# Kernel tuning notes

Measured on AMD Instinct MI355X. Metric: run time of the kernel, lower is better.

Reference implementation:

```python
import jax, jax.numpy as jnp
import numpy as np
import math

IN_C = 768
CA = 384
K1 = (3, 1, 1)
K2 = (1, 3, 3)
K3 = (3, 3, 3)


def _dwconv3d(x, w, b):
    # x: [B, Ca, T, H, W]; w: [Ca, 1, kt, kh, kw]; depthwise (groups = Ca)
    pads = [(k // 2, k // 2) for k in w.shape[2:]]
    y = jax.lax.conv_general_dilated(
        x, w, window_strides=(1, 1, 1), padding=pads,
        feature_group_count=x.shape[1],
        dimension_numbers=("NCDHW", "OIDHW", "NCDHW"))
    return y + b[None, :, None, None, None]


def setup_inputs() -> dict:
    key = jax.random.key(0)
    ks = jax.random.split(key, 12)
    s = 0.02
    x = jax.random.normal(ks[0], (128, 197, IN_C), dtype=jnp.float32)
    fc1_w = jax.random.normal(ks[1], (CA, IN_C), dtype=jnp.float32) * s
    fc1_b = jnp.zeros((CA,), dtype=jnp.float32)
    conv1_w = jax.random.normal(ks[2], (CA, 1) + K1, dtype=jnp.float32) * s
    conv1_b = jax.random.normal(ks[3], (CA,), dtype=jnp.float32) * s
    conv2_w = jax.random.normal(ks[4], (CA, 1) + K2, dtype=jnp.float32) * s
    conv2_b = jax.random.normal(ks[5], (CA,), dtype=jnp.float32) * s
    conv3_w = jax.random.normal(ks[6], (CA, 1) + K3, dtype=jnp.float32) * s
    conv3_b = jax.random.normal(ks[7], (CA,), dtype=jnp.float32) * s
    proj_w = jax.random.normal(ks[8], (CA, 1) + K1, dtype=jnp.float32) * s
    proj_b = jax.random.normal(ks[9], (CA,), dtype=jnp.float32) * s
    fc2_w = jax.random.normal(ks[10], (IN_C, CA), dtype=jnp.float32) * s
    fc2_b = jnp.zeros((IN_C,), dtype=jnp.float32)
    return {
        "x": x, "fc1_w": fc1_w, "fc1_b": fc1_b,
        "conv1_w": conv1_w, "conv1_b": conv1_b,
        "conv2_w": conv2_w, "conv2_b": conv2_b,
        "conv3_w": conv3_w, "conv3_b": conv3_b,
        "proj_w": proj_w, "proj_b": proj_b,
        "fc2_w": fc2_w, "fc2_b": fc2_b,
        "T": 16,
    }


def reference(x, fc1_w, fc1_b, conv1_w, conv1_b, conv2_w, conv2_b,
              conv3_w, conv3_b, proj_w, proj_b, fc2_w, fc2_b, T):
    BT, L, C = x.shape
    B = BT // T
    H = W = round(math.sqrt(L - 1))
    Ca = fc1_w.shape[0]
    x_id = x
    # drop CLS token, project down: [BT, L-1, Ca]
    h = jnp.einsum("blc,ac->bla", x[:, 1:, :], fc1_w) + fc1_b
    # [B, Ca, T, H, W]
    h = h.reshape(B, T, H, W, Ca).transpose(0, 4, 1, 2, 3)
    identity = h
    h = (_dwconv3d(h, conv1_w, conv1_b)
         + _dwconv3d(h, conv2_w, conv2_b)
         + _dwconv3d(h, conv3_w, conv3_b)) / 3.0
    h = h + identity
    h = h + _dwconv3d(h, proj_w, proj_b)
    # back to tokens: [BT, L-1, Ca]
    h = h.transpose(0, 2, 3, 4, 1).reshape(BT, L - 1, Ca)
    h = jnp.einsum("bla,ca->blc", h, fc2_w) + fc2_b
    return x_id.at[:, 1:, :].add(h)
```

## Files before the change

kernel.cpp:

```cpp
#include <hip/hip_runtime.h>
#include <cstdint>

typedef __bf16 bf16_t;
typedef __bf16 bf16x4 __attribute__((ext_vector_type(4)));
typedef __bf16 bf16x8 __attribute__((ext_vector_type(8)));
typedef float f32x4 __attribute__((ext_vector_type(4)));

#define BT_   128
#define LTOK  197
#define CIN   768
#define CA_   384
#define TT    16
#define HH    14
#define NTOK  25088

__device__ __forceinline__ void gl_lds16(const void* g, void* l) {
  __builtin_amdgcn_global_load_lds(
      (const __attribute__((address_space(1))) unsigned int*)g,
      (__attribute__((address_space(3))) unsigned int*)l,
      16, 0, 0);
}

#define SBAR() do { __builtin_amdgcn_sched_barrier(0); \
                    __builtin_amdgcn_s_barrier(); \
                    __builtin_amdgcn_sched_barrier(0); } while (0)

__global__ void prep_weights_kernel(
    const float* __restrict__ c1w, const float* __restrict__ c1b,
    const float* __restrict__ c2w, const float* __restrict__ c2b,
    const float* __restrict__ c3w, const float* __restrict__ c3b,
    const float* __restrict__ projw,
    bf16_t* __restrict__ Wtb,
    float* __restrict__ beff,
    float* __restrict__ pwt) {
  int a = blockIdx.x * blockDim.x + threadIdx.x;
  if (a >= CA_) return;
  for (int dt = 0; dt < 3; dt++)
    for (int dh = 0; dh < 3; dh++)
      for (int dw = 0; dw < 3; dw++) {
        float v = c3w[a*27 + dt*9 + dh*3 + dw];
        if (dh == 1 && dw == 1) v += c1w[a*3 + dt];
        if (dt == 1)            v += c2w[a*9 + dh*3 + dw];
        v *= (1.0f/3.0f);
        if (dt == 1 && dh == 1 && dw == 1) v += 1.0f;
        Wtb[((dt*3+dh)*3+dw)*CA_ + a] = (bf16_t)v;
      }
  beff[a] = (c1b[a] + c2b[a] + c3b[a]) * (1.0f/3.0f);
  pwt[0*CA_ + a] = projw[a*3 + 0];
  pwt[1*CA_ + a] = projw[a*3 + 1];
  pwt[2*CA_ + a] = projw[a*3 + 2];
}

__global__ __launch_bounds__(256) void convert_w_kernel(
    const float* __restrict__ fc1w, const float* __restrict__ fc2w,
    const float* __restrict__ x, float* __restrict__ out,
    bf16_t* __restrict__ W1f, bf16_t* __restrict__ W2f,
    bf16_t* __restrict__ xb) {
  const int NW1 = CA_*CIN/4;
  const int NW2 = CIN*CA_/4;
  const int NX  = BT_*LTOK*CIN/4;
  const int total = NW1 + NW2 + NX;
  for (int i = blockIdx.x*256 + threadIdx.x; i < total; i += gridDim.x*256) {
    if (i < NW1) {
      int e = i*4, f = e >> 9, t = e & 511, l = t >> 3, jb = t & 7;
      int ch = f / 24, cb = f - ch*24;
      int col = cb*16 + (l & 15);
      int k   = ch*32 + ((l >> 4) << 3) + jb;
      float4 v = *(const float4*)(fc1w + (size_t)col*CIN + k);
      bf16x4 b; b[0]=(bf16_t)v.x; b[1]=(bf16_t)v.y; b[2]=(bf16_t)v.z; b[3]=(bf16_t)v.w;
      *(bf16x4*)(W1f + e) = b;
    } else if (i < NW1 + NW2) {
      int e = (i - NW1)*4, f = e >> 9, t = e & 511, l = t >> 3, jb = t & 7;
      int ch = f / 48, cb = f - ch*48;
      int col = cb*16 + (l & 15);
      int k   = ch*32 + ((l >> 4) << 3) + jb;
      float4 v = *(const float4*)(fc2w + (size_t)col*CA_ + k);
      bf16x4 b; b[0]=(bf16_t)v.x; b[1]=(bf16_t)v.y; b[2]=(bf16_t)v.z; b[3]=(bf16_t)v.w;
      *(bf16x4*)(W2f + e) = b;
    } else {
      int j = i - NW1 - NW2;
      int row = j / 192;
      int c4  = j - row*192;
      int l   = row % 197;
      float4 v = ((const float4*)x)[(size_t)j];
      if (l == 0) {
        ((float4*)out)[(size_t)j] = v;
      } else {
        int tok = (row/197)*196 + (l - 1);
        bf16x4 b; b[0]=(bf16_t)v.x; b[1]=(bf16_t)v.y; b[2]=(bf16_t)v.z; b[3]=(bf16_t)v.w;
        *(bf16x4*)(xb + (size_t)tok*CIN + c4*4) = b;
      }
    }
  }
}

__global__ __launch_bounds__(256) void gemm1_kernel(
    const bf16_t* __restrict__ xb, const bf16_t* __restrict__ W1f,
    const float* __restrict__ fc1b, bf16_t* __restrict__ H0) {
  __shared__ bf16_t Alds[3][4096];
  const int tid  = threadIdx.x;
  const int lane = tid & 63;
  const int wave = tid >> 6;
  const int bm = blockIdx.x, bn = blockIdx.y;

  const bf16_t* asrc0 = xb + (size_t)(bm*128 + (tid>>2))*CIN + (tid&3)*8;
  const bf16_t* asrc1 = asrc0 + (size_t)64*CIN;
  const int off0 = tid*8;
  const int off1 = tid*8 + 2048;

  const int quad = lane >> 4;
  const int r16  = lane & 15;
  const int wm = (wave >> 1) * 64;
  const int wn = (wave & 1) * 64;

  const bf16_t* wb = W1f + ((size_t)(bn*8 + (wave & 1)*4))*512 + lane*8;

  f32x4 acc[4][4] = {};

#define G1_A(S, K) do { \
    gl_lds16(asrc0 + (K), &Alds[S][off0]); \
    gl_lds16(asrc1 + (K), &Alds[S][off1]); } while (0)
#define G1_B(CH) do { \
    bfr[0] = *(const bf16x8*)(wb + (size_t)((CH)*24 + 0)*512); \
    bfr[1] = *(const bf16x8*)(wb + (size_t)((CH)*24 + 1)*512); \
    bfr[2] = *(const bf16x8*)(wb + (size_t)((CH)*24 + 2)*512); \
    bfr[3] = *(const bf16x8*)(wb + (size_t)((CH)*24 + 3)*512); } while (0)
#define G1_M(S) do { bf16x8 af_[4]; \
    _Pragma("unroll") \
    for (int mt = 0; mt < 4; mt++) \
      af_[mt] = *(const bf16x8*)&Alds[S][(wm + mt*16 + r16)*32 + quad*8]; \
    _Pragma("unroll") \
    for (int mt = 0; mt < 4; mt++) \
      _Pragma("unroll") \
      for (int nt = 0; nt < 4; nt++) \
        acc[mt][nt] = __builtin_amdgcn_mfma_f32_16x16x32_bf16(af_[mt], bfr[nt], acc[mt][nt], 0, 0, 0); \
  } while (0)

  G1_A(0, 0);
  G1_A(1, 32);
  asm volatile("s_waitcnt vmcnt(2)" ::: "memory");
  SBAR();

  #pragma unroll 1
  for (int ii = 0; ii < 7; ii++) {
    #pragma unroll
    for (int j = 0; j < 3; j++) {
      const int i = ii*3 + j;
      bf16x8 bfr[4];
      G1_B(i);
      __builtin_amdgcn_sched_barrier(0);
      G1_A((j + 2) % 3, (i + 2)*32);
      G1_M(j);
      asm volatile("s_waitcnt vmcnt(2)" ::: "memory");
      SBAR();
    }
  }
  {
    bf16x8 bfr[4];
    G1_B(21);
    __builtin_amdgcn_sched_barrier(0);
    G1_A(2, 23*32);
    G1_M(0);
    asm volatile("s_waitcnt vmcnt(2)" ::: "memory");
    SBAR();
  }
  {
    bf16x8 bfr[4];
    G1_B(22);
    __builtin_amdgcn_sched_barrier(0);
    G1_M(1);
    asm volatile("s_waitcnt vmcnt(0)" ::: "memory");
    SBAR();
  }
  {
    bf16x8 bfr[4];
    G1_B(23);
    G1_M(2);
  }

  #pragma unroll
  for (int nt = 0; nt < 4; nt++) {
    const int col = bn*128 + wn + nt*16 + r16;
    const float bias = fc1b[col];
    #pragma unroll
    for (int mt = 0; mt < 4; mt++) {
      const int row0 = bm*128 + wm + mt*16 + quad*4;
      #pragma unroll
      for (int rg = 0; rg < 4; rg++)
        H0[(size_t)(row0 + rg)*CA_ + col] = (bf16_t)(acc[mt][nt][rg] + bias);
    }
  }
#undef G1_A
#undef G1_B
#undef G1_M
}

__global__ __launch_bounds__(192) void conv_kernel(
    const bf16_t* __restrict__ H0,
    const bf16_t* __restrict__ Wtb,
    const float* __restrict__ beff,
    const float* __restrict__ pwt,
    const float* __restrict__ pb,
    bf16_t* __restrict__ Z) {
  __shared__ bf16_t Wlds[27*CA_];
  __shared__ float  ybuf[2][2][CA_];

  const int tid = threadIdx.x;
  {
    const uint4* src = (const uint4*)Wtb;
    uint4* dst = (uint4*)Wlds;
    #pragma unroll
    for (int i = 0; i < 7; i++) {
      int idx = tid + i*192;
      if (idx < 27*CA_/8) dst[idx] = src[idx];
    }
  }

  const int blk  = blockIdx.x;
  const int b    = blk & 7;
  const int pair = blk >> 3;
  const int cg   = tid % 48;
  const int ct   = tid / 48;
  const int col  = ct >> 1;
  const int th   = ct & 1;
  const int hw   = pair*2 + col;
  const int h    = hw / HH, w = hw % HH;
  const int c0   = cg * 8;
  const int t0   = th * 8;

  float y[8][8];
  {
    f32x4 bv0 = *(const f32x4*)(beff + c0);
    f32x4 bv1 = *(const f32x4*)(beff + c0 + 4);
    #pragma unroll
    for (int i = 0; i < 8; i++) {
      #pragma unroll
      for (int c = 0; c < 4; c++) { y[i][c] = bv0[c]; y[i][c+4] = bv1[c]; }
    }
  }

  __syncthreads();

  const size_t rowstride = (size_t)196*CA_;
  const bf16_t* base_t0 = H0 + ((size_t)(b*TT + t0)*196)*CA_ + c0;
  const int tau_e_off = th ? -1 : 8;

  for (int j = 0; j < 9; j++) {
    const int dh = j / 3, dw = j - dh*3;
    const int h2 = h + dh - 1, w2 = w + dw - 1;
    const bool ok = ((unsigned)h2 < HH) && ((unsigned)w2 < HH);
    const int sp = ok ? (h2*HH + w2) : hw;
    const float m = ok ? 1.0f : 0.0f;

    const bf16x8 wv0 = *(const bf16x8*)&Wlds[(0*9+j)*CA_ + c0];
    const bf16x8 wv1 = *(const bf16x8*)&Wlds[(1*9+j)*CA_ + c0];
    const bf16x8 wv2 = *(const bf16x8*)&Wlds[(2*9+j)*CA_ + c0];
    float mw0[8], mw1[8], mw2[8];
    #pragma unroll
    for (int c = 0; c < 8; c++) {
      mw0[c] = m * (float)wv0[c];
      mw1[c] = m * (float)wv1[c];
      mw2[c] = m * (float)wv2[c];
    }

    const bf16_t* tp = base_t0 + (size_t)sp*CA_;
    bf16x8 gv[8];
    #pragma unroll
    for (int i = 0; i < 8; i++)
      gv[i] = *(const bf16x8*)(tp + (ptrdiff_t)i*(ptrdiff_t)rowstride);
    const bf16x8 ge = *(const bf16x8*)(tp + (ptrdiff_t)tau_e_off*(ptrdiff_t)rowstride);

    #pragma unroll
    for (int i = 0; i < 8; i++) {
      float gf[8];
      #pragma unroll
      for (int c = 0; c < 8; c++) gf[c] = (float)gv[i][c];
      #pragma unroll
      for (int c = 0; c < 8; c++) y[i][c] += gf[c]*mw1[c];
      if (i > 0) {
        #pragma unroll
        for (int c = 0; c < 8; c++) y[i-1][c] += gf[c]*mw2[c];
      }
      if (i < 7) {
        #pragma unroll
        for (int c = 0; c < 8; c++) y[i+1][c] += gf[c]*mw0[c];
      }
    }
    {
      float gf[8];
      #pragma unroll
      for (int c = 0; c < 8; c++) gf[c] = (float)ge[c];
      if (th) {
        #pragma unroll
        for (int c = 0; c < 8; c++) y[0][c] += gf[c]*mw0[c];
      } else {
        #pragma unroll
        for (int c = 0; c < 8; c++) y[7][c] += gf[c]*mw2[c];
      }
    }
  }

  #pragma unroll
  for (int c = 0; c < 8; c++) ybuf[col][th][c0+c] = th ? y[0][c] : y[7][c];
  __syncthreads();
  float yedge[8];
  #pragma unroll
  for (int c = 0; c < 8; c++) yedge[c] = ybuf[col][1-th][c0+c];

  float p0[8], p1[8], p2[8], pbv[8];
  {
    f32x4 a0 = *(const f32x4*)(pwt + 0*CA_ + c0), a1 = *(const f32x4*)(pwt + 0*CA_ + c0 + 4);
    f32x4 b0 = *(const f32x4*)(pwt + 1*CA_ + c0), b1 = *(const f32x4*)(pwt + 1*CA_ + c0 + 4);
    f32x4 d0 = *(const f32x4*)(pwt + 2*CA_ + c0), d1 = *(const f32x4*)(pwt + 2*CA_ + c0 + 4);
    f32x4 e0 = *(const f32x4*)(pb + c0),          e1 = *(const f32x4*)(pb + c0 + 4);
    #pragma unroll
    for (int c = 0; c < 4; c++) {
      p0[c]=a0[c]; p0[c+4]=a1[c];
      p1[c]=b0[c]; p1[c+4]=b1[c];
      p2[c]=d0[c]; p2[c+4]=d1[c];
      pbv[c]=e0[c]; pbv[c+4]=e1[c];
    }
  }

  bf16_t* zbase = Z + ((size_t)(b*TT + t0)*196 + hw)*CA_ + c0;
  #pragma unroll
  for (int i = 0; i < 8; i++) {
    bf16x8 zo;
    #pragma unroll
    for (int c = 0; c < 8; c++) {
      const float ym = (i > 0) ? y[i-1][c] : (th ? yedge[c] : 0.f);
      const float yp = (i < 7) ? y[i+1][c] : (th ? 0.f : yedge[c]);
      const float z  = y[i][c] + pbv[c] + p0[c]*ym + p1[c]*y[i][c] + p2[c]*yp;
      zo[c] = (bf16_t)z;
    }
    *(bf16x8*)(zbase + (size_t)i*rowstride) = zo;
  }
}

__global__ __launch_bounds__(256) void gemm2_kernel(
    const bf16_t* __restrict__ Z, const bf16_t* __restrict__ W2f,
    const float* __restrict__ fc2b, const float* __restrict__ x,
    float* __restrict__ out) {
  __shared__ bf16_t Alds[3][4096];
  const int tid  = threadIdx.x;
  const int lane = tid & 63;
  const int wave = tid >> 6;
  const int bm = blockIdx.x, bn = blockIdx.y;

  const bf16_t* asrc0 = Z + (size_t)(bm*128 + (tid>>2))*CA_ + (tid&3)*8;
  const bf16_t* asrc1 = asrc0 + (size_t)64*CA_;
  const int off0 = tid*8;
  const int off1 = tid*8 + 2048;

  const int quad = lane >> 4;
  const int r16  = lane & 15;
  const int wm = (wave >> 1) * 64;
  const int wn = (wave & 1) * 64;

  const bf16_t* wb = W2f + ((size_t)(bn*8 + (wave & 1)*4))*512 + lane*8;

  f32x4 acc[4][4] = {};

#define G2_A(S, K) do { \
    gl_lds16(asrc0 + (K), &Alds[S][off0]); \
    gl_lds16(asrc1 + (K), &Alds[S][off1]); } while (0)
#define G2_B(CH) do { \
    bfr[0] = *(const bf16x8*)(wb + (size_t)((CH)*48 + 0)*512); \
    bfr[1] = *(const bf16x8*)(wb + (size_t)((CH)*48 + 1)*512); \
    bfr[2] = *(const bf16x8*)(wb + (size_t)((CH)*48 + 2)*512); \
    bfr[3] = *(const bf16x8*)(wb + (size_t)((CH)*48 + 3)*512); } while (0)
#define G2_M(S) do { bf16x8 af_[4]; \
    _Pragma("unroll") \
    for (int mt = 0; mt < 4; mt++) \
      af_[mt] = *(const bf16x8*)&Alds[S][(wm + mt*16 + r16)*32 + quad*8]; \
    _Pragma("unroll") \
    for (int mt = 0; mt < 4; mt++) \
      _Pragma("unroll") \
      for (int nt = 0; nt < 4; nt++) \
        acc[mt][nt] = __builtin_amdgcn_mfma_f32_16x16x32_bf16(af_[mt], bfr[nt], acc[mt][nt], 0, 0, 0); \
  } while (0)

  G2_A(0, 0);
  G2_A(1, 32);
  asm volatile("s_waitcnt vmcnt(2)" ::: "memory");
  SBAR();

  #pragma unroll 1
  for (int ii = 0; ii < 3; ii++) {
    #pragma unroll
    for (int j = 0; j < 3; j++) {
      const int i = ii*3 + j;
      bf16x8 bfr[4];
      G2_B(i);
      __builtin_amdgcn_sched_barrier(0);
      G2_A((j + 2) % 3, (i + 2)*32);
      G2_M(j);
      asm volatile("s_waitcnt vmcnt(2)" ::: "memory");
      SBAR();
    }
  }
  {
    bf16x8 bfr[4];
    G2_B(9);
    __builtin_amdgcn_sched_barrier(0);
    G2_A(2, 11*32);
    G2_M(0);
    asm volatile("s_waitcnt vmcnt(2)" ::: "memory");
    SBAR();
  }
  {
    bf16x8 bfr[4];
    G2_B(10);
    __builtin_amdgcn_sched_barrier(0);
    G2_M(1);
    asm volatile("s_waitcnt vmcnt(0)" ::: "memory");
    SBAR();
  }
  {
    bf16x8 bfr[4];
    G2_B(11);
    G2_M(2);
  }

  #pragma unroll
  for (int nt = 0; nt < 4; nt++) {
    const int col = bn*128 + wn + nt*16 + r16;
    const float bias = fc2b[col];
    #pragma unroll
    for (int mt = 0; mt < 4; mt++) {
      #pragma unroll
      for (int rg = 0; rg < 4; rg++) {
        const int tok = bm*128 + wm + mt*16 + quad*4 + rg;
        const int bt  = tok / 196;
        const size_t o = (size_t)(tok + bt + 1)*CIN + col;
        out[o] = x[o] + acc[mt][nt][rg] + bias;
      }
    }
  }
#undef G2_A
#undef G2_B
#undef G2_M
}

extern "C" void kernel_launch(void* const* d_in, const int* in_sizes, int n_in,
                              void* d_out, int out_size, void* d_ws, size_t ws_size,
                              hipStream_t stream) {
  (void)in_sizes; (void)n_in; (void)out_size; (void)ws_size;
  const float* x    = (const float*)d_in[0];
  const float* fc1w = (const float*)d_in[1];
  const float* fc1b = (const float*)d_in[2];
  const float* c1w  = (const float*)d_in[3];
  const float* c1b  = (const float*)d_in[4];
  const float* c2w  = (const float*)d_in[5];
  const float* c2b  = (const float*)d_in[6];
  const float* c3w  = (const float*)d_in[7];
  const float* c3b  = (const float*)d_in[8];
  const float* pw   = (const float*)d_in[9];
  const float* pb   = (const float*)d_in[10];
  const float* fc2w = (const float*)d_in[11];
  const float* fc2b = (const float*)d_in[12];
  float* out = (float*)d_out;

  char* ws = (char*)d_ws;
  bf16_t* W1f  = (bf16_t*)(ws);
  bf16_t* W2f  = (bf16_t*)(ws + 589824);
  bf16_t* Wtb  = (bf16_t*)(ws + 1179648);
  float*  beff = (float*) (ws + 1200384);
  float*  pwt  = (float*) (ws + 1201920);
  bf16_t* xb   = (bf16_t*)(ws + 1206528);
  bf16_t* Z    = (bf16_t*)(ws + 1206528);
  bf16_t* H0   = (bf16_t*)(ws + 39741696);

  prep_weights_kernel<<<dim3(2), dim3(192), 0, stream>>>(
      c1w, c1b, c2w, c2b, c3w, c3b, pw, Wtb, beff, pwt);
  convert_w_kernel<<<dim3(4096), dim3(256), 0, stream>>>(fc1w, fc2w, x, out, W1f, W2f, xb);
  gemm1_kernel<<<dim3(196, 3), dim3(256), 0, stream>>>(xb, W1f, fc1b, H0);
  conv_kernel<<<dim3(784), dim3(192), 0, stream>>>(H0, Wtb, beff, pwt, pb, Z);
  gemm2_kernel<<<dim3(196, 6), dim3(256), 0, stream>>>(Z, W2f, fc2b, x, out);
}
```

Measured before the change: 266.3 us.

## Shrink GEMM block tiles to 64x128 and fold weight prep into convert kernel

Both GEMM kernels move from a 128x128 block tile (2x2 wave grid, 4x4 MFMA tiles per wave) to a 64x128 tile where each of the four waves owns 64 rows by 32 columns. This doubles the grid to 392 row blocks and halves LDS per block, aiming at better occupancy and load balance across CUs. The cost is more redundant B-weight loads and less A reuse per block. Separately, the small prep_weights kernel is merged into convert_w_kernel to save one launch.

After: 262.6 us. Within noise of the previous version (-1.4%).

```diff
diff --git a/kernel.cpp b/kernel.cpp
--- a/kernel.cpp
+++ b/kernel.cpp
@@ -25,42 +25,40 @@
                     __builtin_amdgcn_s_barrier(); \
                     __builtin_amdgcn_sched_barrier(0); } while (0)
 
-__global__ void prep_weights_kernel(
+__global__ __launch_bounds__(256) void convert_w_kernel(
+    const float* __restrict__ fc1w, const float* __restrict__ fc2w,
+    const float* __restrict__ x, float* __restrict__ out,
+    bf16_t* __restrict__ W1f, bf16_t* __restrict__ W2f,
+    bf16_t* __restrict__ xb,
     const float* __restrict__ c1w, const float* __restrict__ c1b,
     const float* __restrict__ c2w, const float* __restrict__ c2b,
     const float* __restrict__ c3w, const float* __restrict__ c3b,
     const float* __restrict__ projw,
-    bf16_t* __restrict__ Wtb,
-    float* __restrict__ beff,
-    float* __restrict__ pwt) {
-  int a = blockIdx.x * blockDim.x + threadIdx.x;
-  if (a >= CA_) return;
-  for (int dt = 0; dt < 3; dt++)
-    for (int dh = 0; dh < 3; dh++)
-      for (int dw = 0; dw < 3; dw++) {
-        float v = c3w[a*27 + dt*9 + dh*3 + dw];
-        if (dh == 1 && dw == 1) v += c1w[a*3 + dt];
-        if (dt == 1)            v += c2w[a*9 + dh*3 + dw];
-        v *= (1.0f/3.0f);
-        if (dt == 1 && dh == 1 && dw == 1) v += 1.0f;
-        Wtb[((dt*3+dh)*3+dw)*CA_ + a] = (bf16_t)v;
-      }
-  beff[a] = (c1b[a] + c2b[a] + c3b[a]) * (1.0f/3.0f);
-  pwt[0*CA_ + a] = projw[a*3 + 0];
-  pwt[1*CA_ + a] = projw[a*3 + 1];
-  pwt[2*CA_ + a] = projw[a*3 + 2];
-}
-
-__global__ __launch_bounds__(256) void convert_w_kernel(
-    const float* __restrict__ fc1w, const float* __restrict__ fc2w,
-    const float* __restrict__ x, float* __restrict__ out,
-    bf16_t* __restrict__ W1f, bf16_t* __restrict__ W2f,
-    bf16_t* __restrict__ xb) {
+    bf16_t* __restrict__ Wtb, float* __restrict__ beff, float* __restrict__ pwt) {
+  const int gid = blockIdx.x*256 + threadIdx.x;
+  if (gid < CA_) {
+    const int a = gid;
+    for (int dt = 0; dt < 3; dt++)
+      for (int dh = 0; dh < 3; dh++)
+        for (int dw = 0; dw < 3; dw++) {
+          float v = c3w[a*27 + dt*9 + dh*3 + dw];
+          if (dh == 1 && dw == 1) v += c1w[a*3 + dt];
+          if (dt == 1)            v += c2w[a*9 + dh*3 + dw];
+          v *= (1.0f/3.0f);
+          if (dt == 1 && dh == 1 && dw == 1) v += 1.0f;
+          Wtb[((dt*3+dh)*3+dw)*CA_ + a] = (bf16_t)v;
+        }
+    beff[a] = (c1b[a] + c2b[a] + c3b[a]) * (1.0f/3.0f);
+    pwt[0*CA_ + a] = projw[a*3 + 0];
+    pwt[1*CA_ + a] = projw[a*3 + 1];
+    pwt[2*CA_ + a] = projw[a*3 + 2];
+  }
+
   const int NW1 = CA_*CIN/4;
   const int NW2 = CIN*CA_/4;
   const int NX  = BT_*LTOK*CIN/4;
   const int total = NW1 + NW2 + NX;
-  for (int i = blockIdx.x*256 + threadIdx.x; i < total; i += gridDim.x*256) {
+  for (int i = gid; i < total; i += gridDim.x*256) {
     if (i < NW1) {
       int e = i*4, f = e >> 9, t = e & 511, l = t >> 3, jb = t & 7;
       int ch = f / 24, cb = f - ch*24;
@@ -97,48 +95,40 @@
 __global__ __launch_bounds__(256) void gemm1_kernel(
     const bf16_t* __restrict__ xb, const bf16_t* __restrict__ W1f,
     const float* __restrict__ fc1b, bf16_t* __restrict__ H0) {
-  __shared__ bf16_t Alds[3][4096];
+  __shared__ bf16_t Alds[3][2048];
   const int tid  = threadIdx.x;
   const int lane = tid & 63;
   const int wave = tid >> 6;
   const int bm = blockIdx.x, bn = blockIdx.y;
 
-  const bf16_t* asrc0 = xb + (size_t)(bm*128 + (tid>>2))*CIN + (tid&3)*8;
-  const bf16_t* asrc1 = asrc0 + (size_t)64*CIN;
-  const int off0 = tid*8;
-  const int off1 = tid*8 + 2048;
+  const bf16_t* asrc = xb + (size_t)(bm*64 + (tid>>2))*CIN + (tid&3)*8;
+  const int aoff = tid*8;
 
   const int quad = lane >> 4;
   const int r16  = lane & 15;
-  const int wm = (wave >> 1) * 64;
-  const int wn = (wave & 1) * 64;
-
-  const bf16_t* wb = W1f + ((size_t)(bn*8 + (wave & 1)*4))*512 + lane*8;
-
-  f32x4 acc[4][4] = {};
-
-#define G1_A(S, K) do { \
-    gl_lds16(asrc0 + (K), &Alds[S][off0]); \
-    gl_lds16(asrc1 + (K), &Alds[S][off1]); } while (0)
+
+  const bf16_t* wb = W1f + ((size_t)(bn*8 + wave*2))*512 + lane*8;
+
+  f32x4 acc[4][2] = {};
+
+#define G1_A(S, K) gl_lds16(asrc + (K), &Alds[S][aoff])
 #define G1_B(CH) do { \
     bfr[0] = *(const bf16x8*)(wb + (size_t)((CH)*24 + 0)*512); \
-    bfr[1] = *(const bf16x8*)(wb + (size_t)((CH)*24 + 1)*512); \
-    bfr[2] = *(const bf16x8*)(wb + (size_t)((CH)*24 + 2)*512); \
-    bfr[3] = *(const bf16x8*)(wb + (size_t)((CH)*24 + 3)*512); } while (0)
+    bfr[1] = *(const bf16x8*)(wb + (size_t)((CH)*24 + 1)*512); } while (0)
 #define G1_M(S) do { bf16x8 af_[4]; \
     _Pragma("unroll") \
     for (int mt = 0; mt < 4; mt++) \
-      af_[mt] = *(const bf16x8*)&Alds[S][(wm + mt*16 + r16)*32 + quad*8]; \
+      af_[mt] = *(const bf16x8*)&Alds[S][(mt*16 + r16)*32 + quad*8]; \
     _Pragma("unroll") \
     for (int mt = 0; mt < 4; mt++) \
       _Pragma("unroll") \
-      for (int nt = 0; nt < 4; nt++) \
+      for (int nt = 0; nt < 2; nt++) \
         acc[mt][nt] = __builtin_amdgcn_mfma_f32_16x16x32_bf16(af_[mt], bfr[nt], acc[mt][nt], 0, 0, 0); \
   } while (0)
 
   G1_A(0, 0);
   G1_A(1, 32);
-  asm volatile("s_waitcnt vmcnt(2)" ::: "memory");
+  asm volatile("s_waitcnt vmcnt(1)" ::: "memory");
   SBAR();
 
   #pragma unroll 1
@@ -146,26 +136,26 @@
     #pragma unroll
     for (int j = 0; j < 3; j++) {
       const int i = ii*3 + j;
-      bf16x8 bfr[4];
+      bf16x8 bfr[2];
       G1_B(i);
       __builtin_amdgcn_sched_barrier(0);
       G1_A((j + 2) % 3, (i + 2)*32);
       G1_M(j);
-      asm volatile("s_waitcnt vmcnt(2)" ::: "memory");
+      asm volatile("s_waitcnt vmcnt(1)" ::: "memory");
       SBAR();
     }
   }
   {
-    bf16x8 bfr[4];
+    bf16x8 bfr[2];
     G1_B(21);
     __builtin_amdgcn_sched_barrier(0);
     G1_A(2, 23*32);
     G1_M(0);
-    asm volatile("s_waitcnt vmcnt(2)" ::: "memory");
+    asm volatile("s_waitcnt vmcnt(1)" ::: "memory");
     SBAR();
   }
   {
-    bf16x8 bfr[4];
+    bf16x8 bfr[2];
     G1_B(22);
     __builtin_amdgcn_sched_barrier(0);
     G1_M(1);
@@ -173,18 +163,18 @@
     SBAR();
   }
   {
-    bf16x8 bfr[4];
+    bf16x8 bfr[2];
     G1_B(23);
     G1_M(2);
   }
 
   #pragma unroll
-  for (int nt = 0; nt < 4; nt++) {
-    const int col = bn*128 + wn + nt*16 + r16;
+  for (int nt = 0; nt < 2; nt++) {
+    const int col = bn*128 + wave*32 + nt*16 + r16;
     const float bias = fc1b[col];
     #pragma unroll
     for (int mt = 0; mt < 4; mt++) {
-      const int row0 = bm*128 + wm + mt*16 + quad*4;
+      const int row0 = bm*64 + mt*16 + quad*4;
       #pragma unroll
       for (int rg = 0; rg < 4; rg++)
         H0[(size_t)(row0 + rg)*CA_ + col] = (bf16_t)(acc[mt][nt][rg] + bias);
@@ -341,48 +331,40 @@
     const bf16_t* __restrict__ Z, const bf16_t* __restrict__ W2f,
     const float* __restrict__ fc2b, const float* __restrict__ x,
     float* __restrict__ out) {
-  __shared__ bf16_t Alds[3][4096];
+  __shared__ bf16_t Alds[3][2048];
   const int tid  = threadIdx.x;
   const int lane = tid & 63;
   const int wave = tid >> 6;
   const int bm = blockIdx.x, bn = blockIdx.y;
 
-  const bf16_t* asrc0 = Z + (size_t)(bm*128 + (tid>>2))*CA_ + (tid&3)*8;
-  const bf16_t* asrc1 = asrc0 + (size_t)64*CA_;
-  const int off0 = tid*8;
-  const int off1 = tid*8 + 2048;
+  const bf16_t* asrc = Z + (size_t)(bm*64 + (tid>>2))*CA_ + (tid&3)*8;
+  const int aoff = tid*8;
 
   const int quad = lane >> 4;
   const int r16  = lane & 15;
-  const int wm = (wave >> 1) * 64;
-  const int wn = (wave & 1) * 64;
-
-  const bf16_t* wb = W2f + ((size_t)(bn*8 + (wave & 1)*4))*512 + lane*8;
-
-  f32x4 acc[4][4] = {};
-
-#define G2_A(S, K) do { \
-    gl_lds16(asrc0 + (K), &Alds[S][off0]); \
-    gl_lds16(asrc1 + (K), &Alds[S][off1]); } while (0)
+
+  const bf16_t* wb = W2f + ((size_t)(bn*8 + wave*2))*512 + lane*8;
+
+  f32x4 acc[4][2] = {};
+
+#define G2_A(S, K) gl_lds16(asrc + (K), &Alds[S][aoff])
 #define G2_B(CH) do { \
     bfr[0] = *(const bf16x8*)(wb + (size_t)((CH)*48 + 0)*512); \
-    bfr[1] = *(const bf16x8*)(wb + (size_t)((CH)*48 + 1)*512); \
-    bfr[2] = *(const bf16x8*)(wb + (size_t)((CH)*48 + 2)*512); \
-    bfr[3] = *(const bf16x8*)(wb + (size_t)((CH)*48 + 3)*512); } while (0)
+    bfr[1] = *(const bf16x8*)(wb + (size_t)((CH)*48 + 1)*512); } while (0)
 #define G2_M(S) do { bf16x8 af_[4]; \
     _Pragma("unroll") \
     for (int mt = 0; mt < 4; mt++) \
-      af_[mt] = *(const bf16x8*)&Alds[S][(wm + mt*16 + r16)*32 + quad*8]; \
+      af_[mt] = *(const bf16x8*)&Alds[S][(mt*16 + r16)*32 + quad*8]; \
     _Pragma("unroll") \
     for (int mt = 0; mt < 4; mt++) \
       _Pragma("unroll") \
-      for (int nt = 0; nt < 4; nt++) \
+      for (int nt = 0; nt < 2; nt++) \
         acc[mt][nt] = __builtin_amdgcn_mfma_f32_16x16x32_bf16(af_[mt], bfr[nt], acc[mt][nt], 0, 0, 0); \
   } while (0)
 
   G2_A(0, 0);
   G2_A(1, 32);
-  asm volatile("s_waitcnt vmcnt(2)" ::: "memory");
+  asm volatile("s_waitcnt vmcnt(1)" ::: "memory");
   SBAR();
 
   #pragma unroll 1
@@ -390,26 +372,26 @@
     #pragma unroll
     for (int j = 0; j < 3; j++) {
       const int i = ii*3 + j;
-      bf16x8 bfr[4];
+      bf16x8 bfr[2];
       G2_B(i);
       __builtin_amdgcn_sched_barrier(0);
       G2_A((j + 2) % 3, (i + 2)*32);
       G2_M(j);
-      asm volatile("s_waitcnt vmcnt(2)" ::: "memory");
+      asm volatile("s_waitcnt vmcnt(1)" ::: "memory");
       SBAR();
     }
   }
   {
-    bf16x8 bfr[4];
+    bf16x8 bfr[2];
     G2_B(9);
     __builtin_amdgcn_sched_barrier(0);
     G2_A(2, 11*32);
     G2_M(0);
-    asm volatile("s_waitcnt vmcnt(2)" ::: "memory");
+    asm volatile("s_waitcnt vmcnt(1)" ::: "memory");
     SBAR();
   }
   {
-    bf16x8 bfr[4];
+    bf16x8 bfr[2];
     G2_B(10);
     __builtin_amdgcn_sched_barrier(0);
     G2_M(1);
@@ -417,20 +399,20 @@
     SBAR();
   }
   {
-    bf16x8 bfr[4];
+    bf16x8 bfr[2];
     G2_B(11);
     G2_M(2);
   }
 
   #pragma unroll
-  for (int nt = 0; nt < 4; nt++) {
-    const int col = bn*128 + wn + nt*16 + r16;
+  for (int nt = 0; nt < 2; nt++) {
+    const int col = bn*128 + wave*32 + nt*16 + r16;
     const float bias = fc2b[col];
     #pragma unroll
     for (int mt = 0; mt < 4; mt++) {
       #pragma unroll
       for (int rg = 0; rg < 4; rg++) {
-        const int tok = bm*128 + wm + mt*16 + quad*4 + rg;
+        const int tok = bm*64 + mt*16 + quad*4 + rg;
         const int bt  = tok / 196;
         const size_t o = (size_t)(tok + bt + 1)*CIN + col;
         out[o] = x[o] + acc[mt][nt][rg] + bias;
@@ -471,10 +453,10 @@
   bf16_t* Z    = (bf16_t*)(ws + 1206528);
   bf16_t* H0   = (bf16_t*)(ws + 39741696);
 
-  prep_weights_kernel<<<dim3(2), dim3(192), 0, stream>>>(
+  convert_w_kernel<<<dim3(4096), dim3(256), 0, stream>>>(
+      fc1w, fc2w, x, out, W1f, W2f, xb,
       c1w, c1b, c2w, c2b, c3w, c3b, pw, Wtb, beff, pwt);
-  convert_w_kernel<<<dim3(4096), dim3(256), 0, stream>>>(fc1w, fc2w, x, out, W1f, W2f, xb);
-  gemm1_kernel<<<dim3(196, 3), dim3(256), 0, stream>>>(xb, W1f, fc1b, H0);
+  gemm1_kernel<<<dim3(392, 3), dim3(256), 0, stream>>>(xb, W1f, fc1b, H0);
   conv_kernel<<<dim3(784), dim3(192), 0, stream>>>(H0, Wtb, beff, pwt, pb, Z);
-  gemm2_kernel<<<dim3(196, 6), dim3(256), 0, stream>>>(Z, W2f, fc2b, x, out);
-}
+  gemm2_kernel<<<dim3(392, 6), dim3(256), 0, stream>>>(Z, W2f, fc2b, x, out);
+}
```
